# Kernel optimization log

Measured on AMD Instinct MI355X. Metric: run time of the kernel, lower is better.

Reference implementation:

```python
import jax, jax.numpy as jnp
import numpy as np

N_NODES = 50000
N_EDGES = 600000
D = 128
NUM_LAYERS = 2
ALPHA = 0.5
EPS = 1e-12  # torch F.normalize eps


def setup_inputs() -> dict:
    key = jax.random.key(0)
    k1, k2, k3, k4, k5 = jax.random.split(key, 5)
    x = jax.random.normal(k1, (N_NODES, D), dtype=jnp.float32)
    edge_attr = jax.random.normal(k2, (N_EDGES, D), dtype=jnp.float32)
    question_emb = jax.random.normal(k3, (D,), dtype=jnp.float32)
    src = jax.random.randint(k4, (N_EDGES,), 0, N_NODES)
    dst = jax.random.randint(k5, (N_EDGES,), 0, N_NODES)
    edge_index = jnp.stack([src, dst], axis=0).astype(jnp.int64)
    return {"x": x, "edge_attr": edge_attr, "question_emb": question_emb, "edge_index": edge_index}


def reference(x, edge_attr, question_emb, edge_index):
    num_nodes = x.shape[0]
    # edge similarity: cosine of edge_attr rows vs question vector
    ea = edge_attr / jnp.maximum(jnp.linalg.norm(edge_attr, axis=1, keepdims=True), EPS)
    q = question_emb / jnp.maximum(jnp.linalg.norm(question_emb), EPS)
    edge_sim = ea @ q  # [E]
    src, dst = edge_index[0], edge_index[1]
    # degree of destination nodes (constant across layers)
    deg = jax.ops.segment_sum(jnp.ones_like(edge_sim), dst, num_segments=num_nodes)
    deg = jnp.clip(deg, 1.0)[:, None]  # [N,1]
    for _ in range(NUM_LAYERS):
        msgs = x[src] * edge_sim[:, None]                              # [E,D] gather + scale
        x_new = jax.ops.segment_sum(msgs, dst, num_segments=num_nodes)  # [N,D] scatter-add
        x_new = x_new / deg                                             # mean aggregation
        x = ALPHA * x + (1.0 - ALPHA) * x_new                           # residual blend
    return x
```

## Files before the change

### kernel.cpp

```cpp
#include <hip/hip_runtime.h>
#include <math.h>

#define N_NODES 50000
#define N_EDGES 600000
#define D 128
#define EPS 1e-12f

#define SCAN_B 256
#define N_SCAN_BLOCKS ((N_NODES + SCAN_B - 1) / SCAN_B)

__global__ void qnorm_kernel(const float* __restrict__ q, float* __restrict__ qn) {
    __shared__ float red[2];
    int t = threadIdx.x;
    float v = q[t];
    float ss = v * v;
    #pragma unroll
    for (int off = 32; off > 0; off >>= 1) ss += __shfl_down(ss, off);
    if ((t & 63) == 0) red[t >> 6] = ss;
    __syncthreads();
    float inv = 1.0f / fmaxf(sqrtf(red[0] + red[1]), EPS);
    qn[t] = v * inv;
}

__global__ void edge_sim_kernel(const float* __restrict__ ea,
                                const float* __restrict__ qn,
                                const int* __restrict__ dst,
                                float* __restrict__ sim,
                                int* __restrict__ cnt) {
    int gid  = blockIdx.x * blockDim.x + threadIdx.x;
    int wave = gid >> 6;
    if (wave >= N_EDGES / 2) return;
    int lane = threadIdx.x & 63;
    int half = lane >> 5;
    int l32  = lane & 31;
    int e    = 2 * wave + half;

    float4 v = ((const float4*)(ea + (size_t)e * D))[l32];
    float4 q = ((const float4*)qn)[l32];
    float dot = v.x * q.x + v.y * q.y + v.z * q.z + v.w * q.w;
    float ss  = v.x * v.x + v.y * v.y + v.z * v.z + v.w * v.w;
    #pragma unroll
    for (int off = 16; off > 0; off >>= 1) {
        dot += __shfl_xor(dot, off);
        ss  += __shfl_xor(ss, off);
    }
    if (l32 == 0) {
        sim[e] = dot / fmaxf(sqrtf(ss), EPS);
        atomicAdd(&cnt[dst[e]], 1);
    }
}

__global__ void block_sum_kernel(const int* __restrict__ cnt, int* __restrict__ bsum) {
    __shared__ int s[SCAN_B];
    int t = threadIdx.x;
    int i = blockIdx.x * SCAN_B + t;
    s[t] = (i < N_NODES) ? cnt[i] : 0;
    __syncthreads();
    for (int off = SCAN_B / 2; off > 0; off >>= 1) {
        if (t < off) s[t] += s[t + off];
        __syncthreads();
    }
    if (t == 0) bsum[blockIdx.x] = s[0];
}

__global__ void scan_bsums_kernel(int* __restrict__ bsum) {
    __shared__ int s[SCAN_B];
    int t = threadIdx.x;
    int v = (t < N_SCAN_BLOCKS) ? bsum[t] : 0;
    s[t] = v;
    __syncthreads();
    for (int off = 1; off < SCAN_B; off <<= 1) {
        int a = (t >= off) ? s[t - off] : 0;
        __syncthreads();
        s[t] += a;
        __syncthreads();
    }
    if (t < N_SCAN_BLOCKS) bsum[t] = s[t] - v;
}

__global__ void scan_final_kernel(const int* __restrict__ cnt,
                                  const int* __restrict__ bsum,
                                  int* __restrict__ row_ptr,
                                  int* __restrict__ cursor,
                                  float* __restrict__ deg_inv) {
    __shared__ int s[SCAN_B];
    int t = threadIdx.x;
    int i = blockIdx.x * SCAN_B + t;
    int v = (i < N_NODES) ? cnt[i] : 0;
    s[t] = v;
    __syncthreads();
    for (int off = 1; off < SCAN_B; off <<= 1) {
        int a = (t >= off) ? s[t - off] : 0;
        __syncthreads();
        s[t] += a;
        __syncthreads();
    }
    if (i < N_NODES) {
        int rp = s[t] - v + bsum[blockIdx.x];
        row_ptr[i] = rp;
        cursor[i]  = rp;
        deg_inv[i] = 1.0f / fmaxf((float)v, 1.0f);
    }
    if (i == N_NODES - 1) row_ptr[N_NODES] = N_EDGES;
}

__global__ void fill_kernel(const int* __restrict__ src, const int* __restrict__ dst,
                            const float* __restrict__ sim,
                            int* __restrict__ cursor,
                            int* __restrict__ csr_src, float* __restrict__ csr_sim) {
    int e = blockIdx.x * blockDim.x + threadIdx.x;
    if (e >= N_EDGES) return;
    int d = dst[e];
    int idx = atomicAdd(&cursor[d], 1);
    csr_src[idx] = src[e];
    csr_sim[idx] = sim[e];
}

__global__ void agg_kernel(const float* __restrict__ xin,
                           const int* __restrict__ row_ptr,
                           const int* __restrict__ csr_src,
                           const float* __restrict__ csr_sim,
                           const float* __restrict__ deg_inv,
                           float* __restrict__ xout) {
    int gid  = blockIdx.x * blockDim.x + threadIdx.x;
    int node = gid >> 6;
    if (node >= N_NODES) return;
    int lane = threadIdx.x & 63;
    int half = lane >> 5;
    int l32  = lane & 31;

    int beg = row_ptr[node];
    int end = row_ptr[node + 1];
    int n   = end - beg;

    int   sl = 0; float wl = 0.0f;
    if (lane < n) { sl = csr_src[beg + lane]; wl = csr_sim[beg + lane]; }

    float4 acc = make_float4(0.0f, 0.0f, 0.0f, 0.0f);
    int nn = (n < 64) ? n : 64;
    #pragma unroll 2
    for (int j = half; j < nn; j += 2) {
        int   s = __shfl(sl, j);
        float w = __shfl(wl, j);
        float4 v = ((const float4*)(xin + (size_t)s * D))[l32];
        acc.x += v.x * w; acc.y += v.y * w; acc.z += v.z * w; acc.w += v.w * w;
    }
    for (int j = 64 + half; j < n; j += 2) {
        int   s = csr_src[beg + j];
        float w = csr_sim[beg + j];
        float4 v = ((const float4*)(xin + (size_t)s * D))[l32];
        acc.x += v.x * w; acc.y += v.y * w; acc.z += v.z * w; acc.w += v.w * w;
    }
    acc.x += __shfl_xor(acc.x, 32);
    acc.y += __shfl_xor(acc.y, 32);
    acc.z += __shfl_xor(acc.z, 32);
    acc.w += __shfl_xor(acc.w, 32);

    if (half == 0) {
        float di = deg_inv[node];
        float4 a = ((const float4*)(xin + (size_t)node * D))[l32];
        float4 o;
        o.x = 0.5f * a.x + 0.5f * acc.x * di;
        o.y = 0.5f * a.y + 0.5f * acc.y * di;
        o.z = 0.5f * a.z + 0.5f * acc.z * di;
        o.w = 0.5f * a.w + 0.5f * acc.w * di;
        ((float4*)(xout + (size_t)node * D))[l32] = o;
    }
}

extern "C" void kernel_launch(void* const* d_in, const int* in_sizes, int n_in,
                              void* d_out, int out_size, void* d_ws, size_t ws_size,
                              hipStream_t stream) {
    const float* x  = (const float*)d_in[0];
    const float* ea = (const float*)d_in[1];
    const float* q  = (const float*)d_in[2];
    const int*   ei = (const int*)d_in[3];
    const int* src = ei;
    const int* dst = ei + N_EDGES;
    float* out = (float*)d_out;

    float* x1       = (float*)d_ws;
    float* sim      = x1 + (size_t)N_NODES * D;
    float* csr_sim  = sim + N_EDGES;
    float* deg_inv  = csr_sim + N_EDGES;
    float* qn       = deg_inv + N_NODES;
    int*   cnt      = (int*)(qn + 128);
    int*   row_ptr  = cnt + N_NODES;
    int*   cursor   = row_ptr + N_NODES + 1;
    int*   bsum     = cursor + N_NODES;
    int*   csr_src  = bsum + 256;

    hipMemsetAsync(cnt, 0, (size_t)N_NODES * sizeof(int), stream);

    qnorm_kernel<<<1, 128, 0, stream>>>(q, qn);

    {
        long long threads = (long long)(N_EDGES / 2) * 64;
        int blocks = (int)((threads + 255) / 256);
        edge_sim_kernel<<<blocks, 256, 0, stream>>>(ea, qn, dst, sim, cnt);
    }

    block_sum_kernel<<<N_SCAN_BLOCKS, SCAN_B, 0, stream>>>(cnt, bsum);
    scan_bsums_kernel<<<1, SCAN_B, 0, stream>>>(bsum);
    scan_final_kernel<<<N_SCAN_BLOCKS, SCAN_B, 0, stream>>>(cnt, bsum, row_ptr, cursor, deg_inv);

    fill_kernel<<<(N_EDGES + 255) / 256, 256, 0, stream>>>(src, dst, sim, cursor, csr_src, csr_sim);

    const int agg_blocks = (int)(((long long)N_NODES * 64 + 255) / 256);
    agg_kernel<<<agg_blocks, 256, 0, stream>>>(x,  row_ptr, csr_src, csr_sim, deg_inv, x1);
    agg_kernel<<<agg_blocks, 256, 0, stream>>>(x1, row_ptr, csr_src, csr_sim, deg_inv, out);
}
```

Measured before the change: 563.9 us.

## Process two nodes per wave in aggregation, pack CSR entries, fuse qnorm

Aggregation now gives each half-wave its own destination node instead of splitting one node's edges across both halves. That removes the cross-half reduction and halves the number of waves launched, but each half-wave now walks the full edge list serially. CSR source index and weight are packed into one int2 array, so one load fetches both. The question-vector normalization is folded into edge_sim_kernel, with each block recomputing the norm in shared memory, which removes one kernel launch.

```diff
diff --git a/kernel.cpp b/kernel.cpp
--- a/kernel.cpp
+++ b/kernel.cpp
@@ -9,35 +9,36 @@
 #define SCAN_B 256
 #define N_SCAN_BLOCKS ((N_NODES + SCAN_B - 1) / SCAN_B)
 
-__global__ void qnorm_kernel(const float* __restrict__ q, float* __restrict__ qn) {
-    __shared__ float red[2];
-    int t = threadIdx.x;
-    float v = q[t];
-    float ss = v * v;
-    #pragma unroll
-    for (int off = 32; off > 0; off >>= 1) ss += __shfl_down(ss, off);
-    if ((t & 63) == 0) red[t >> 6] = ss;
-    __syncthreads();
-    float inv = 1.0f / fmaxf(sqrtf(red[0] + red[1]), EPS);
-    qn[t] = v * inv;
-}
-
 __global__ void edge_sim_kernel(const float* __restrict__ ea,
-                                const float* __restrict__ qn,
+                                const float* __restrict__ q,
                                 const int* __restrict__ dst,
                                 float* __restrict__ sim,
                                 int* __restrict__ cnt) {
-    int gid  = blockIdx.x * blockDim.x + threadIdx.x;
+    __shared__ float qsh[D];
+    __shared__ float ssh[2];
+    int t = threadIdx.x;
+    if (t < D) {
+        float v = q[t];
+        qsh[t] = v;
+        float ss = v * v;
+        #pragma unroll
+        for (int off = 32; off > 0; off >>= 1) ss += __shfl_down(ss, off);
+        if ((t & 63) == 0) ssh[t >> 6] = ss;
+    }
+    __syncthreads();
+    float qinv = 1.0f / fmaxf(sqrtf(ssh[0] + ssh[1]), EPS);
+
+    int gid  = blockIdx.x * blockDim.x + t;
     int wave = gid >> 6;
     if (wave >= N_EDGES / 2) return;
-    int lane = threadIdx.x & 63;
+    int lane = t & 63;
     int half = lane >> 5;
     int l32  = lane & 31;
     int e    = 2 * wave + half;
 
-    float4 v = ((const float4*)(ea + (size_t)e * D))[l32];
-    float4 q = ((const float4*)qn)[l32];
-    float dot = v.x * q.x + v.y * q.y + v.z * q.z + v.w * q.w;
+    float4 v  = ((const float4*)(ea + (size_t)e * D))[l32];
+    float4 qv = ((const float4*)qsh)[l32];
+    float dot = v.x * qv.x + v.y * qv.y + v.z * qv.z + v.w * qv.w;
     float ss  = v.x * v.x + v.y * v.y + v.z * v.z + v.w * v.w;
     #pragma unroll
     for (int off = 16; off > 0; off >>= 1) {
@@ -45,7 +46,7 @@
         ss  += __shfl_xor(ss, off);
     }
     if (l32 == 0) {
-        sim[e] = dot / fmaxf(sqrtf(ss), EPS);
+        sim[e] = (dot * qinv) / fmaxf(sqrtf(ss), EPS);
         atomicAdd(&cnt[dst[e]], 1);
     }
 }
@@ -106,66 +107,58 @@
 
 __global__ void fill_kernel(const int* __restrict__ src, const int* __restrict__ dst,
                             const float* __restrict__ sim,
-                            int* __restrict__ cursor,
-                            int* __restrict__ csr_src, float* __restrict__ csr_sim) {
+                            int* __restrict__ cursor, int2* __restrict__ csr) {
     int e = blockIdx.x * blockDim.x + threadIdx.x;
     if (e >= N_EDGES) return;
-    int d = dst[e];
-    int idx = atomicAdd(&cursor[d], 1);
-    csr_src[idx] = src[e];
-    csr_sim[idx] = sim[e];
+    int idx = atomicAdd(&cursor[dst[e]], 1);
+    csr[idx] = make_int2(src[e], __float_as_int(sim[e]));
 }
 
 __global__ void agg_kernel(const float* __restrict__ xin,
                            const int* __restrict__ row_ptr,
-                           const int* __restrict__ csr_src,
-                           const float* __restrict__ csr_sim,
+                           const int2* __restrict__ csr,
                            const float* __restrict__ deg_inv,
                            float* __restrict__ xout) {
     int gid  = blockIdx.x * blockDim.x + threadIdx.x;
-    int node = gid >> 6;
-    if (node >= N_NODES) return;
+    int wave = gid >> 6;
     int lane = threadIdx.x & 63;
     int half = lane >> 5;
     int l32  = lane & 31;
+    int node = wave * 2 + half;
+    if (node >= N_NODES) return;
 
     int beg = row_ptr[node];
     int end = row_ptr[node + 1];
     int n   = end - beg;
 
-    int   sl = 0; float wl = 0.0f;
-    if (lane < n) { sl = csr_src[beg + lane]; wl = csr_sim[beg + lane]; }
+    int2 ce = make_int2(0, 0);
+    if (l32 < n) ce = csr[beg + l32];
 
     float4 acc = make_float4(0.0f, 0.0f, 0.0f, 0.0f);
-    int nn = (n < 64) ? n : 64;
-    #pragma unroll 2
-    for (int j = half; j < nn; j += 2) {
-        int   s = __shfl(sl, j);
-        float w = __shfl(wl, j);
+    int nn = (n < 32) ? n : 32;
+    int base = half << 5;
+    #pragma unroll 4
+    for (int j = 0; j < nn; ++j) {
+        int   s = __shfl(ce.x, base + j);
+        float w = __int_as_float(__shfl(ce.y, base + j));
         float4 v = ((const float4*)(xin + (size_t)s * D))[l32];
         acc.x += v.x * w; acc.y += v.y * w; acc.z += v.z * w; acc.w += v.w * w;
     }
-    for (int j = 64 + half; j < n; j += 2) {
-        int   s = csr_src[beg + j];
-        float w = csr_sim[beg + j];
-        float4 v = ((const float4*)(xin + (size_t)s * D))[l32];
+    for (int j = 32; j < n; ++j) {
+        int2 e2 = csr[beg + j];
+        float w = __int_as_float(e2.y);
+        float4 v = ((const float4*)(xin + (size_t)e2.x * D))[l32];
         acc.x += v.x * w; acc.y += v.y * w; acc.z += v.z * w; acc.w += v.w * w;
     }
-    acc.x += __shfl_xor(acc.x, 32);
-    acc.y += __shfl_xor(acc.y, 32);
-    acc.z += __shfl_xor(acc.z, 32);
-    acc.w += __shfl_xor(acc.w, 32);
-
-    if (half == 0) {
-        float di = deg_inv[node];
-        float4 a = ((const float4*)(xin + (size_t)node * D))[l32];
-        float4 o;
-        o.x = 0.5f * a.x + 0.5f * acc.x * di;
-        o.y = 0.5f * a.y + 0.5f * acc.y * di;
-        o.z = 0.5f * a.z + 0.5f * acc.z * di;
-        o.w = 0.5f * a.w + 0.5f * acc.w * di;
-        ((float4*)(xout + (size_t)node * D))[l32] = o;
-    }
+
+    float di = deg_inv[node];
+    float4 a = ((const float4*)(xin + (size_t)node * D))[l32];
+    float4 o;
+    o.x = 0.5f * a.x + 0.5f * acc.x * di;
+    o.y = 0.5f * a.y + 0.5f * acc.y * di;
+    o.z = 0.5f * a.z + 0.5f * acc.z * di;
+    o.w = 0.5f * a.w + 0.5f * acc.w * di;
+    ((float4*)(xout + (size_t)node * D))[l32] = o;
 }
 
 extern "C" void kernel_launch(void* const* d_in, const int* in_sizes, int n_in,
@@ -180,33 +173,30 @@
     float* out = (float*)d_out;
 
     float* x1       = (float*)d_ws;
-    float* sim      = x1 + (size_t)N_NODES * D;
-    float* csr_sim  = sim + N_EDGES;
-    float* deg_inv  = csr_sim + N_EDGES;
-    float* qn       = deg_inv + N_NODES;
-    int*   cnt      = (int*)(qn + 128);
+    int2*  csr      = (int2*)(x1 + (size_t)N_NODES * D);
+    float* sim      = (float*)(csr + N_EDGES);
+    float* deg_inv  = sim + N_EDGES;
+    int*   cnt      = (int*)(deg_inv + N_NODES);
     int*   row_ptr  = cnt + N_NODES;
     int*   cursor   = row_ptr + N_NODES + 1;
     int*   bsum     = cursor + N_NODES;
-    int*   csr_src  = bsum + 256;
 
     hipMemsetAsync(cnt, 0, (size_t)N_NODES * sizeof(int), stream);
-
-    qnorm_kernel<<<1, 128, 0, stream>>>(q, qn);
 
     {
         long long threads = (long long)(N_EDGES / 2) * 64;
         int blocks = (int)((threads + 255) / 256);
-        edge_sim_kernel<<<blocks, 256, 0, stream>>>(ea, qn, dst, sim, cnt);
+        edge_sim_kernel<<<blocks, 256, 0, stream>>>(ea, q, dst, sim, cnt);
     }
 
     block_sum_kernel<<<N_SCAN_BLOCKS, SCAN_B, 0, stream>>>(cnt, bsum);
     scan_bsums_kernel<<<1, SCAN_B, 0, stream>>>(bsum);
     scan_final_kernel<<<N_SCAN_BLOCKS, SCAN_B, 0, stream>>>(cnt, bsum, row_ptr, cursor, deg_inv);
 
-    fill_kernel<<<(N_EDGES + 255) / 256, 256, 0, stream>>>(src, dst, sim, cursor, csr_src, csr_sim);
-
-    const int agg_blocks = (int)(((long long)N_NODES * 64 + 255) / 256);
-    agg_kernel<<<agg_blocks, 256, 0, stream>>>(x,  row_ptr, csr_src, csr_sim, deg_inv, x1);
-    agg_kernel<<<agg_blocks, 256, 0, stream>>>(x1, row_ptr, csr_src, csr_sim, deg_inv, out);
-}
+    fill_kernel<<<(N_EDGES + 255) / 256, 256, 0, stream>>>(src, dst, sim, cursor, csr);
+
+    const long long agg_threads = (long long)((N_NODES + 1) / 2) * 64;
+    const int agg_blocks = (int)((agg_threads + 255) / 256);
+    agg_kernel<<<agg_blocks, 256, 0, stream>>>(x,  row_ptr, csr, deg_inv, x1);
+    agg_kernel<<<agg_blocks, 256, 0, stream>>>(x1, row_ptr, csr, deg_inv, out);
+}
```

After: 572.2 us. Within noise of the previous version (+1.5%).
